# Optimization experiments

Hardware: AMD Instinct MI355X
Metric: run time of the kernel (lower is better)

Reference implementation:

```python
import jax, jax.numpy as jnp
import numpy as np

N, E, G = 250000, 2500000, 512
DIN, H, DEC = 6, 32, 16
BN_EPS = 1e-5


def setup_inputs() -> dict:
    key = jax.random.key(0)
    ks = iter(jax.random.split(key, 64))

    def nrm(shape, s=0.2):
        return s * jax.random.normal(next(ks), shape, jnp.float32)

    inp = {}
    inp["x"] = jax.random.normal(next(ks), (N, DIN), jnp.float32)
    inp["edge_index"] = jax.random.randint(next(ks), (2, E), 0, N)
    inp["batch"] = jnp.sort(jax.random.randint(next(ks), (N,), 0, G))
    dims = [(DIN, H), (H, H), (H, H)]
    for l, (din, dout) in enumerate(dims, 1):
        for d in ("f", "b"):
            inp[f"g{d}{l}_W1"] = nrm((din, dout))
            inp[f"g{d}{l}_b1"] = jnp.zeros((dout,), jnp.float32)
            inp[f"g{d}{l}_W2"] = nrm((dout, dout))
            inp[f"g{d}{l}_b2"] = jnp.zeros((dout,), jnp.float32)
        inp[f"bn{l}_g"] = jnp.ones((dout,), jnp.float32)
        inp[f"bn{l}_b"] = jnp.zeros((dout,), jnp.float32)
    inp["lb_W"] = nrm((H, DEC))
    inp["lb_b"] = jnp.zeros((DEC,), jnp.float32)
    inp["lm_W"] = nrm((DEC, 1))
    inp["lm_b"] = jnp.zeros((1,), jnp.float32)
    return inp


def _gin(x, src, dst, W1, b1, W2, b2):
    # PyG GINConv (eps=0): nn(x + sum_{j->i} x_j); messages flow src -> dst
    agg = jax.ops.segment_sum(x[src], dst, num_segments=x.shape[0])  # [N, d]
    h = x + agg
    return jnp.maximum(h @ W1 + b1, 0.0) @ W2 + b2


def _dgin(x, src, dst, pf, pb, gamma, beta):
    o1 = jax.nn.relu(_gin(x, src, dst, *pf))          # forward direction (A)
    o2 = jax.nn.relu(_gin(x, dst, src, *pb))          # reverse direction (A^T)
    o = 0.5 * (o1 + o2)
    mu = o.mean(0)
    var = o.var(0)  # biased var, as torch BatchNorm1d normalization
    return (o - mu) * jax.lax.rsqrt(var + BN_EPS) * gamma + beta


def reference(x, edge_index, batch,
              gf1_W1, gf1_b1, gf1_W2, gf1_b2, gb1_W1, gb1_b1, gb1_W2, gb1_b2, bn1_g, bn1_b,
              gf2_W1, gf2_b1, gf2_W2, gf2_b2, gb2_W1, gb2_b1, gb2_W2, gb2_b2, bn2_g, bn2_b,
              gf3_W1, gf3_b1, gf3_W2, gf3_b2, gb3_W1, gb3_b1, gb3_W2, gb3_b2, bn3_g, bn3_b,
              lb_W, lb_b, lm_W, lm_b):
    src, dst = edge_index[0], edge_index[1]
    h = _dgin(x, src, dst, (gf1_W1, gf1_b1, gf1_W2, gf1_b2), (gb1_W1, gb1_b1, gb1_W2, gb1_b2), bn1_g, bn1_b)
    h = _dgin(h, src, dst, (gf2_W1, gf2_b1, gf2_W2, gf2_b2), (gb2_W1, gb2_b1, gb2_W2, gb2_b2), bn2_g, bn2_b)
    h = _dgin(h, src, dst, (gf3_W1, gf3_b1, gf3_W2, gf3_b2), (gb3_W1, gb3_b1, gb3_W2, gb3_b2), bn3_g, bn3_b)
    # global mean pool over graphs
    sums = jax.ops.segment_sum(h, batch, num_segments=G)                     # [G, H]
    cnts = jax.ops.segment_sum(jnp.ones((h.shape[0],), h.dtype), batch, num_segments=G)
    pooled = sums / jnp.maximum(cnts, 1.0)[:, None]
    emb = jax.nn.relu(pooled @ lb_W + lb_b)   # dropout: identity (eval)
    return jax.nn.sigmoid(emb @ lm_W + lm_b)  # [G, 1]
```

## Files before the change

kernel.cpp:

```cpp
#include <hip/hip_runtime.h>
#include <math.h>

#define N_NODES 250000
#define N_EDGES 2500000
#define N_GRAPHS 512
#define BN_EPS 1e-5f
#define NT 500000
#define INV_N (1.0f / (float)N_NODES)
#define NBUCK 245
#define BSHIFT 10

__device__ __forceinline__ unsigned short f2bf(float x) {
    unsigned int u = __float_as_uint(x);
    unsigned int r = (u + 0x7FFFu + ((u >> 16) & 1u)) >> 16;
    return (unsigned short)r;
}
__device__ __forceinline__ float bf2f(unsigned short b) {
    return __uint_as_float(((unsigned int)b) << 16);
}


__global__ __launch_bounds__(256)
void k_histA(const int* __restrict__ src, const int* __restrict__ dst,
             int* __restrict__ gcnt, int E)
{
    __shared__ int hF[256], hB[256];
    int t = threadIdx.x;
    hF[t] = 0; hB[t] = 0;
    __syncthreads();
    for (int e = blockIdx.x * 256 + t; e < E; e += gridDim.x * 256) {
        atomicAdd(&hF[dst[e] >> BSHIFT], 1);
        atomicAdd(&hB[src[e] >> BSHIFT], 1);
    }
    __syncthreads();
    if (hF[t]) atomicAdd(&gcnt[t], hF[t]);
    if (hB[t]) atomicAdd(&gcnt[256 + t], hB[t]);
}

__global__ void k_scanBk(const int* __restrict__ gcnt,
                         int* __restrict__ bOffF, int* __restrict__ bOffB,
                         int* __restrict__ cursF, int* __restrict__ cursB,
                         int* __restrict__ off)
{
    __shared__ int s[512];
    int t = threadIdx.x;
    int vF = (t < NBUCK) ? gcnt[t] : 0;
    int vB = (t < NBUCK) ? gcnt[256 + t] : 0;
    s[t] = vF; s[256 + t] = vB;
    __syncthreads();
    for (int o = 1; o < 256; o <<= 1) {
        int xF = (t >= o) ? s[t - o] : 0;
        int xB = (t >= o) ? s[256 + t - o] : 0;
        __syncthreads();
        s[t] += xF; s[256 + t] += xB;
        __syncthreads();
    }
    int exF = s[t] - vF;
    int exB = s[256 + t] - vB;
    if (t < NBUCK) {
        bOffF[t] = exF; cursF[t] = exF;
        bOffB[t] = exB; cursB[t] = exB;
    }
    if (t == 0) {
        bOffF[NBUCK] = N_EDGES;
        bOffB[NBUCK] = N_EDGES;
        off[NT] = 2 * N_EDGES;
    }
}

__global__ __launch_bounds__(256)
void k_scatA(const int* __restrict__ src, const int* __restrict__ dst,
             int* __restrict__ cursF, int* __restrict__ cursB,
             unsigned int* __restrict__ payF, unsigned int* __restrict__ payB, int E)
{
    __shared__ int hF[256], hB[256];
    __shared__ int cF[256], cB[256];
    int t = threadIdx.x;
    hF[t] = 0; hB[t] = 0;
    __syncthreads();
    int e0 = blockIdx.x * 256 + t, STR = gridDim.x * 256;
    for (int e = e0; e < E; e += STR) {
        atomicAdd(&hF[dst[e] >> BSHIFT], 1);
        atomicAdd(&hB[src[e] >> BSHIFT], 1);
    }
    __syncthreads();
    int baseF = 0, baseB = 0;
    if (t < NBUCK) {
        if (hF[t]) baseF = atomicAdd(&cursF[t], hF[t]);
        if (hB[t]) baseB = atomicAdd(&cursB[t], hB[t]);
    }
    __syncthreads();
    cF[t] = baseF; cB[t] = baseB;
    __syncthreads();
    for (int e = e0; e < E; e += STR) {
        int s = src[e], d = dst[e];
        int tf = atomicAdd(&cF[d >> BSHIFT], 1);
        payF[tf] = ((unsigned int)(d & 1023) << 18) | (unsigned int)s;
        int tb = atomicAdd(&cB[s >> BSHIFT], 1);
        payB[tb] = ((unsigned int)(s & 1023) << 18) | (unsigned int)d;
    }
}

__global__ __launch_bounds__(256)
void k_bucket(const unsigned int* __restrict__ payF, const unsigned int* __restrict__ payB,
              const int* __restrict__ bOffF, const int* __restrict__ bOffB,
              int* __restrict__ eidx, int* __restrict__ off)
{
    __shared__ int cnt[1024];
    __shared__ int ps[256];
    int blk = blockIdx.x;
    int d  = (blk >= NBUCK) ? 1 : 0;
    int bb = blk - d * NBUCK;
    const unsigned int* pay = d ? payB : payF;
    const int* bOff = d ? bOffB : bOffF;
    int t = threadIdx.x;
    int lo = bOff[bb], hi = bOff[bb + 1];

    #pragma unroll
    for (int k = 0; k < 4; k++) cnt[t + 256 * k] = 0;
    __syncthreads();
    for (int e = lo + t; e < hi; e += 256)
        atomicAdd(&cnt[pay[e] >> 18], 1);
    __syncthreads();

    int b4 = 4 * t;
    int v0 = cnt[b4], v1 = cnt[b4 + 1], v2 = cnt[b4 + 2], v3 = cnt[b4 + 3];
    int tsum = v0 + v1 + v2 + v3;
    ps[t] = tsum;
    __syncthreads();
    for (int o = 1; o < 256; o <<= 1) {
        int x = (t >= o) ? ps[t - o] : 0;
        __syncthreads();
        ps[t] += x;
        __syncthreads();
    }
    int run = ps[t] - tsum;
    int l0 = run, l1 = run + v0, l2 = run + v0 + v1, l3 = run + v0 + v1 + v2;
    cnt[b4] = l0; cnt[b4 + 1] = l1; cnt[b4 + 2] = l2; cnt[b4 + 3] = l3;

    int gbase = d * N_EDGES + lo;
    int node0 = bb * 1024 + b4;
    if (node0 + 0 < N_NODES) off[d * N_NODES + node0 + 0] = gbase + l0;
    if (node0 + 1 < N_NODES) off[d * N_NODES + node0 + 1] = gbase + l1;
    if (node0 + 2 < N_NODES) off[d * N_NODES + node0 + 2] = gbase + l2;
    if (node0 + 3 < N_NODES) off[d * N_NODES + node0 + 3] = gbase + l3;
    __syncthreads();

    for (int e = lo + t; e < hi; e += 256) {
        unsigned int p = pay[e];
        int r = atomicAdd(&cnt[p >> 18], 1);
        eidx[gbase + r] = (int)(p & 0x3FFFFu);
    }
}


__global__ void pad_x(const float* __restrict__ x, float* __restrict__ xpad, int n)
{
    int i = blockIdx.x * blockDim.x + threadIdx.x;
    if (i >= n * 4) return;
    int node = i >> 2, p2 = i & 3;
    float2 v;
    v.x = (2 * p2     < 6) ? x[node * 6 + 2 * p2]     : 0.f;
    v.y = (2 * p2 + 1 < 6) ? x[node * 6 + 2 * p2 + 1] : 0.f;
    *(float2*)(xpad + node * 8 + 2 * p2) = v;
}


__global__ __launch_bounds__(256, 8)
void gather6p(const float* __restrict__ xpad, const int* __restrict__ off,
              const int* __restrict__ eidx, float* __restrict__ agg, int ngroups)
{
    int tid = threadIdx.x;
    int p2   = tid & 3;
    int slot = tid >> 2;
    for (int grp = blockIdx.x; grp < ngroups; grp += gridDim.x) {
        int node = grp * 64 + slot;
        bool nvalid = (node < N_NODES);
        int nd = nvalid ? node : 0;
        #pragma unroll
        for (int dir = 0; dir < 2; dir++) {
            int u = dir * N_NODES + nd;
            int k0 = off[u], k1 = off[u + 1];
            if (!nvalid) k1 = k0;
            float a0=0.f,a1=0.f,b0=0.f,b1=0.f,c0=0.f,c1=0.f,d0=0.f,d1=0.f;
            for (int p = k0; p < k1; p += 8) {
                #pragma unroll
                for (int q = 0; q < 8; q++) {
                    int kk = p + q;
                    bool act = (kk < k1);
                    int j = eidx[act ? kk : k0];
                    float2 v = *(const float2*)(xpad + j * 8 + 2 * p2);
                    float lo = act ? v.x : 0.f;
                    float hi = act ? v.y : 0.f;
                    if ((q & 3) == 0)      { a0 += lo; a1 += hi; }
                    else if ((q & 3) == 1) { b0 += lo; b1 += hi; }
                    else if ((q & 3) == 2) { c0 += lo; c1 += hi; }
                    else                   { d0 += lo; d1 += hi; }
                }
            }
            if (nvalid && p2 < 3) {
                float2 s;
                s.x = (a0 + b0) + (c0 + d0);
                s.y = (a1 + b1) + (c1 + d1);
                *(float2*)(agg + nd * 12 + dir * 6 + 2 * p2) = s;
            }
        }
    }
}


__global__ __launch_bounds__(256, 8)
void gather16(const unsigned short* __restrict__ xb, const int* __restrict__ off,
              const int* __restrict__ eidx, float* __restrict__ agg, int ngroups)
{
    const unsigned int* xu = (const unsigned int*)xb;
    int tid = threadIdx.x;
    int fp = tid & 15;
    int gg = tid >> 4;
    for (int grp = blockIdx.x; grp < ngroups; grp += gridDim.x) {
        int node = grp * 16 + gg;
        #pragma unroll
        for (int dir = 0; dir < 2; dir++) {
            int u = dir * N_NODES + node;
            int k0 = off[u], k1 = off[u + 1];
            float a0 = 0.f, a1 = 0.f, b0 = 0.f, b1 = 0.f;
            float c0 = 0.f, c1 = 0.f, d0 = 0.f, d1 = 0.f;
            for (int p = k0; p < k1; p += 8) {
                #pragma unroll
                for (int q = 0; q < 8; q++) {
                    int kk = p + q;
                    bool act = (kk < k1);
                    int j = eidx[act ? kk : k0];
                    unsigned int v = xu[j * 16 + fp];
                    float lo = act ? __uint_as_float(v << 16) : 0.f;
                    float hi = act ? __uint_as_float(v & 0xFFFF0000u) : 0.f;
                    if ((q & 3) == 0)      { a0 += lo; a1 += hi; }
                    else if ((q & 3) == 1) { b0 += lo; b1 += hi; }
                    else if ((q & 3) == 2) { c0 += lo; c1 += hi; }
                    else                   { d0 += lo; d1 += hi; }
                }
            }
            float2 s;
            s.x = (a0 + b0) + (c0 + d0);
            s.y = (a1 + b1) + (c1 + d1);
            *(float2*)(agg + node * 64 + dir * 32 + 2 * fp) = s;
        }
    }
}


__global__ __launch_bounds__(256, 6)
void gather16_12(const unsigned short* __restrict__ xb, const int* __restrict__ off,
                 const int* __restrict__ eidx, float* __restrict__ agg, int ngroups)
{
    const unsigned int* xu = (const unsigned int*)xb;
    int tid = threadIdx.x;
    int fp = tid & 15;
    int gg = tid >> 4;
    for (int grp = blockIdx.x; grp < ngroups; grp += gridDim.x) {
        int node = grp * 16 + gg;
        #pragma unroll
        for (int dir = 0; dir < 2; dir++) {
            int u = dir * N_NODES + node;
            int k0 = off[u], k1 = off[u + 1];
            float a0 = 0.f, a1 = 0.f, b0 = 0.f, b1 = 0.f;
            float c0 = 0.f, c1 = 0.f, d0 = 0.f, d1 = 0.f;
            for (int p = k0; p < k1; p += 12) {
                #pragma unroll
                for (int q = 0; q < 12; q++) {
                    int kk = p + q;
                    bool act = (kk < k1);
                    int j = eidx[act ? kk : k0];
                    unsigned int v = xu[j * 16 + fp];
                    float lo = act ? __uint_as_float(v << 16) : 0.f;
                    float hi = act ? __uint_as_float(v & 0xFFFF0000u) : 0.f;
                    if ((q & 3) == 0)      { a0 += lo; a1 += hi; }
                    else if ((q & 3) == 1) { b0 += lo; b1 += hi; }
                    else if ((q & 3) == 2) { c0 += lo; c1 += hi; }
                    else                   { d0 += lo; d1 += hi; }
                }
            }
            float2 s;
            s.x = (a0 + b0) + (c0 + d0);
            s.y = (a1 + b1) + (c1 + d1);
            *(float2*)(agg + node * 64 + dir * 32 + 2 * fp) = s;
        }
    }
}


template <int DIN, bool BN_IN, bool IN_BF16>
__global__ __launch_bounds__(256, 2)
void dgin_mlp2(const void* __restrict__ xin_v, const float* __restrict__ agg,
               const int* __restrict__ off,
               const float* __restrict__ in_stats,
               const float* __restrict__ in_g, const float* __restrict__ in_b,
               const float* __restrict__ W1f, const float* __restrict__ b1f,
               const float* __restrict__ W2f, const float* __restrict__ b2f,
               const float* __restrict__ W1b, const float* __restrict__ b1b,
               const float* __restrict__ W2b, const float* __restrict__ b2b,
               unsigned short* __restrict__ out, float* __restrict__ stats, int n)
{
    const float* xf = (const float*)xin_v;
    const unsigned short* xb = (const unsigned short*)xin_v;

    __shared__ __align__(16) float sW1[2][DIN * 32];
    __shared__ __align__(16) float sW2[2][32 * 32];
    __shared__ float sb1[2][32], sb2[2][32];
    __shared__ float sscale[32], sshift[32];
    __shared__ float sred[4 * 64];

    int tid = threadIdx.x;
    for (int i = tid; i < DIN * 32; i += 256) { sW1[0][i] = W1f[i]; sW1[1][i] = W1b[i]; }
    for (int i = tid; i < 32 * 32;  i += 256) { sW2[0][i] = W2f[i]; sW2[1][i] = W2b[i]; }
    if (tid < 32) {
        sb1[0][tid] = b1f[tid]; sb1[1][tid] = b1b[tid];
        sb2[0][tid] = b2f[tid]; sb2[1][tid] = b2b[tid];
        if (BN_IN) {
            float mu  = in_stats[tid] * INV_N;
            float var = in_stats[32 + tid] * INV_N - mu * mu;
            float sc  = in_g[tid] * rsqrtf(var + BN_EPS);
            sscale[tid] = sc;
            sshift[tid] = in_b[tid] - mu * sc;
        } else { sscale[tid] = 1.f; sshift[tid] = 0.f; }
    }
    __syncthreads();

    int n0 = blockIdx.x * 256 + tid;
    bool valid = (n0 < n);
    int node = valid ? n0 : (n - 1);

    float xr[DIN];
    if (IN_BF16) {
        const uint4* xp = (const uint4*)(xb + node * 32);
        #pragma unroll
        for (int q = 0; q < 4; q++) {
            uint4 u = xp[q];
            unsigned int w[4] = {u.x, u.y, u.z, u.w};
            #pragma unroll
            for (int k = 0; k < 4; k++) {
                xr[8*q + 2*k]     = __uint_as_float(w[k] << 16);
                xr[8*q + 2*k + 1] = __uint_as_float(w[k] & 0xFFFF0000u);
            }
        }
    } else if (DIN == 32) {
        const float4* xp = (const float4*)(xf + node * 32);
        #pragma unroll
        for (int q = 0; q < 8; q++) {
            float4 w = xp[q];
            xr[4*q+0] = w.x; xr[4*q+1] = w.y; xr[4*q+2] = w.z; xr[4*q+3] = w.w;
        }
    } else {
        const float2* xp = (const float2*)(xf + node * DIN);
        #pragma unroll
        for (int q = 0; q < DIN / 2; q++) {
            float2 w = xp[q];
            xr[2*q+0] = w.x; xr[2*q+1] = w.y;
        }
    }

    float o[32];

    #pragma unroll
    for (int dir = 0; dir < 2; dir++) {
        float ag[DIN];
        if (DIN == 32) {
            const float4* ap = (const float4*)(agg + node * 64 + dir * 32);
            #pragma unroll
            for (int q = 0; q < 8; q++) {
                float4 w = ap[q];
                ag[4*q+0] = w.x; ag[4*q+1] = w.y; ag[4*q+2] = w.z; ag[4*q+3] = w.w;
            }
        } else {
            const float* ap = agg + node * (2 * DIN) + dir * DIN;
            #pragma unroll
            for (int i = 0; i < DIN; i++) ag[i] = ap[i];
        }
        int ob = dir * N_NODES + node;
        float degp1 = (float)(off[ob + 1] - off[ob] + 1);

        float t1[32];
        #pragma unroll
        for (int j = 0; j < 32; j++) t1[j] = sb1[dir][j];
        #pragma unroll
        for (int i = 0; i < DIN; i++) {
            float hv = xr[i] + ag[i];
            if (BN_IN) hv = fmaf(sscale[i], hv, degp1 * sshift[i]);
            const float4* wr = (const float4*)(&sW1[dir][i * 32]);
            #pragma unroll
            for (int q = 0; q < 8; q++) {
                float4 w = wr[q];
                t1[4*q+0] = fmaf(hv, w.x, t1[4*q+0]);
                t1[4*q+1] = fmaf(hv, w.y, t1[4*q+1]);
                t1[4*q+2] = fmaf(hv, w.z, t1[4*q+2]);
                t1[4*q+3] = fmaf(hv, w.w, t1[4*q+3]);
            }
        }
        #pragma unroll
        for (int j = 0; j < 32; j++) t1[j] = fmaxf(t1[j], 0.f);

        float o2[32];
        #pragma unroll
        for (int j = 0; j < 32; j++) o2[j] = sb2[dir][j];
        #pragma unroll
        for (int i = 0; i < 32; i++) {
            float hv = t1[i];
            const float4* wr = (const float4*)(&sW2[dir][i * 32]);
            #pragma unroll
            for (int q = 0; q < 8; q++) {
                float4 w = wr[q];
                o2[4*q+0] = fmaf(hv, w.x, o2[4*q+0]);
                o2[4*q+1] = fmaf(hv, w.y, o2[4*q+1]);
                o2[4*q+2] = fmaf(hv, w.z, o2[4*q+2]);
                o2[4*q+3] = fmaf(hv, w.w, o2[4*q+3]);
            }
        }
        if (dir == 0) {
            #pragma unroll
            for (int j = 0; j < 32; j++) o[j] = fmaxf(o2[j], 0.f);
        } else {
            #pragma unroll
            for (int j = 0; j < 32; j++) o[j] = 0.5f * (o[j] + fmaxf(o2[j], 0.f));
        }
    }

    #pragma unroll
    for (int j = 0; j < 32; j++) o[j] = bf2f(f2bf(o[j]));

    if (valid) {
        uint4* op = (uint4*)(out + node * 32);
        #pragma unroll
        for (int q = 0; q < 4; q++) {
            uint4 u;
            u.x = (unsigned int)f2bf(o[8*q+0]) | ((unsigned int)f2bf(o[8*q+1]) << 16);
            u.y = (unsigned int)f2bf(o[8*q+2]) | ((unsigned int)f2bf(o[8*q+3]) << 16);
            u.z = (unsigned int)f2bf(o[8*q+4]) | ((unsigned int)f2bf(o[8*q+5]) << 16);
            u.w = (unsigned int)f2bf(o[8*q+6]) | ((unsigned int)f2bf(o[8*q+7]) << 16);
            op[q] = u;
        }
    }

    int lane = tid & 63;
    int wave = tid >> 6;
    #pragma unroll
    for (int f = 0; f < 32; f++) {
        float v = valid ? o[f] : 0.f;
        float v2 = v * v;
        #pragma unroll
        for (int offs = 32; offs > 0; offs >>= 1) {
            v  += __shfl_down(v, offs);
            v2 += __shfl_down(v2, offs);
        }
        if (lane == 0) {
            sred[wave * 64 + f]      = v;
            sred[wave * 64 + 32 + f] = v2;
        }
    }
    __syncthreads();
    if (tid < 64) {
        float a = sred[tid] + sred[64 + tid] + sred[128 + tid] + sred[192 + tid];
        atomicAdd(&stats[tid], a);
    }
}


__global__ void pool_seg(const unsigned short* __restrict__ h, const int* __restrict__ batch,
                         float* __restrict__ psum, float* __restrict__ pcnt, int n)
{
    int tid = threadIdx.x;
    int grp = tid >> 5, f = tid & 31;
    int base = blockIdx.x * 256;
    float acc = 0.f, cnt = 0.f;
    int curg = -1;
    for (int it = 0; it < 32; it++) {
        int nd = base + grp + it * 8;
        if (nd < n) {
            int g = batch[nd];
            if (g != curg) {
                if (curg >= 0) {
                    atomicAdd(&psum[curg * 32 + f], acc);
                    if (f == 0) atomicAdd(&pcnt[curg], cnt);
                }
                curg = g; acc = 0.f; cnt = 0.f;
            }
            acc += bf2f(h[nd * 32 + f]);
            cnt += 1.f;
        }
    }
    if (curg >= 0) {
        atomicAdd(&psum[curg * 32 + f], acc);
        if (f == 0) atomicAdd(&pcnt[curg], cnt);
    }
}

__global__ void head_kernel(const float* __restrict__ psum, const float* __restrict__ pcnt,
                            const float* __restrict__ stats3,
                            const float* __restrict__ g3, const float* __restrict__ b3,
                            const float* __restrict__ lbW, const float* __restrict__ lbb,
                            const float* __restrict__ lmW, const float* __restrict__ lmb,
                            float* __restrict__ out)
{
    int g = threadIdx.x;
    float cnt = fmaxf(pcnt[g], 1.0f);
    float inv = 1.0f / cnt;
    float p[32];
    #pragma unroll
    for (int i = 0; i < 32; i++) {
        float mu  = stats3[i] * INV_N;
        float var = stats3[32 + i] * INV_N - mu * mu;
        float a   = g3[i] * rsqrtf(var + BN_EPS);
        float b   = b3[i] - mu * a;
        p[i] = fmaf(a, psum[g * 32 + i] * inv, b);
    }
    float z = lmb[0];
    #pragma unroll
    for (int k = 0; k < 16; k++) {
        float acc = lbb[k];
        #pragma unroll
        for (int i = 0; i < 32; i++) acc += p[i] * lbW[i * 16 + k];
        z += fmaxf(acc, 0.0f) * lmW[k];
    }
    out[g] = 1.0f / (1.0f + expf(-z));
}


extern "C" void kernel_launch(void* const* d_in, const int* in_sizes, int n_in,
                              void* d_out, int out_size, void* d_ws, size_t ws_size,
                              hipStream_t stream)
{
    const float* x   = (const float*)d_in[0];
    const int* ei    = (const int*)d_in[1];
    const int* batch = (const int*)d_in[2];
    const int* src = ei;
    const int* dst = ei + N_EDGES;
    char* ws = (char*)d_ws;

    auto W = [&](int l, int j) { return (const float*)d_in[3 + (l - 1) * 10 + j]; };

    unsigned short* h = (unsigned short*)(ws + 0);
    float* xpad = (float*)(ws + 16000016);
    float* agg  = (float*)(ws + 32000000);
    int*   eidx = (int*)  (ws + 96000000);
    int*   off  = (int*)  (ws + 116000000);
    int* gcnt  = (int*)(ws + 32000000);
    int* bOffF = (int*)(ws + 32002048);
    int* bOffB = (int*)(ws + 32003072);
    int* cursF = (int*)(ws + 32004096);
    int* cursB = (int*)(ws + 32005120);
    unsigned int* payF = (unsigned int*)(ws + 32008192);
    unsigned int* payB = (unsigned int*)(ws + 42008192);
    float* stats1 = (float*)(ws + 118000016);
    float* stats2 = stats1 + 64;
    float* stats3 = stats1 + 128;
    float* psum   = (float*)(ws + 118000784);
    float* pcnt   = (float*)(ws + 118066320);

    hipMemsetAsync(gcnt, 0, 2048, stream);
    k_histA<<<1024, 256, 0, stream>>>(src, dst, gcnt, N_EDGES);
    k_scanBk<<<1, 256, 0, stream>>>(gcnt, bOffF, bOffB, cursF, cursB, off);
    k_scatA<<<384, 256, 0, stream>>>(src, dst, cursF, cursB, payF, payB, N_EDGES);
    k_bucket<<<2 * NBUCK, 256, 0, stream>>>(payF, payB, bOffF, bOffB, eidx, off);

    pad_x<<<(N_NODES * 4 + 255) / 256, 256, 0, stream>>>(x, xpad, N_NODES);
    hipMemsetAsync(stats1, 0, 3 * 64 * 4, stream);

    const int GG   = 4096;
    const int NG64 = (N_NODES + 63) / 64;
    const int NG16 = N_NODES / 16;
    const int GM   = (N_NODES + 255) / 256;

    gather6p<<<GG, 256, 0, stream>>>(xpad, off, eidx, agg, NG64);
    dgin_mlp2<6, false, false><<<GM, 256, 0, stream>>>(
        x, agg, off, nullptr, nullptr, nullptr,
        W(1,0), W(1,1), W(1,2), W(1,3), W(1,4), W(1,5), W(1,6), W(1,7),
        h, stats1, N_NODES);

    gather16<<<GG, 256, 0, stream>>>(h, off, eidx, agg, NG16);
    dgin_mlp2<32, true, true><<<GM, 256, 0, stream>>>(
        h, agg, off, stats1, W(1,8), W(1,9),
        W(2,0), W(2,1), W(2,2), W(2,3), W(2,4), W(2,5), W(2,6), W(2,7),
        h, stats2, N_NODES);

    gather16_12<<<GG, 256, 0, stream>>>(h, off, eidx, agg, NG16);
    dgin_mlp2<32, true, true><<<GM, 256, 0, stream>>>(
        h, agg, off, stats2, W(2,8), W(2,9),
        W(3,0), W(3,1), W(3,2), W(3,3), W(3,4), W(3,5), W(3,6), W(3,7),
        h, stats3, N_NODES);

    hipMemsetAsync(psum, 0, (size_t)N_GRAPHS * 32 * 4, stream);
    hipMemsetAsync(pcnt, 0, (size_t)N_GRAPHS * 4, stream);
    pool_seg<<<(N_NODES + 255) / 256, 256, 0, stream>>>(h, batch, psum, pcnt, N_NODES);
    head_kernel<<<1, 512, 0, stream>>>(psum, pcnt, stats3, W(3,8), W(3,9),
        (const float*)d_in[33], (const float*)d_in[34],
        (const float*)d_in[35], (const float*)d_in[36],
        (float*)d_out);
}
```

Baseline: 808.1 us.

## Split forward and reverse MLP directions across paired threads in dgin_mlp2

```diff
diff --git a/kernel.cpp b/kernel.cpp
--- a/kernel.cpp
+++ b/kernel.cpp
@@ -290,7 +290,7 @@
 
 
 template <int DIN, bool BN_IN, bool IN_BF16>
-__global__ __launch_bounds__(256, 2)
+__global__ __launch_bounds__(256, 4)
 void dgin_mlp2(const void* __restrict__ xin_v, const float* __restrict__ agg,
                const int* __restrict__ off,
                const float* __restrict__ in_stats,
@@ -326,7 +326,9 @@
     }
     __syncthreads();
 
-    int n0 = blockIdx.x * 256 + tid;
+    int nl  = tid >> 1;
+    int dir = tid & 1;
+    int n0 = blockIdx.x * 128 + nl;
     bool valid = (n0 < n);
     int node = valid ? n0 : (n - 1);
 
@@ -343,13 +345,6 @@
                 xr[8*q + 2*k + 1] = __uint_as_float(w[k] & 0xFFFF0000u);
             }
         }
-    } else if (DIN == 32) {
-        const float4* xp = (const float4*)(xf + node * 32);
-        #pragma unroll
-        for (int q = 0; q < 8; q++) {
-            float4 w = xp[q];
-            xr[4*q+0] = w.x; xr[4*q+1] = w.y; xr[4*q+2] = w.z; xr[4*q+3] = w.w;
-        }
     } else {
         const float2* xp = (const float2*)(xf + node * DIN);
         #pragma unroll
@@ -359,69 +354,65 @@
         }
     }
 
+    float ag[DIN];
+    if (DIN == 32) {
+        const float4* ap = (const float4*)(agg + node * 64 + dir * 32);
+        #pragma unroll
+        for (int q = 0; q < 8; q++) {
+            float4 w = ap[q];
+            ag[4*q+0] = w.x; ag[4*q+1] = w.y; ag[4*q+2] = w.z; ag[4*q+3] = w.w;
+        }
+    } else {
+        const float* ap = agg + node * (2 * DIN) + dir * DIN;
+        #pragma unroll
+        for (int i = 0; i < DIN; i++) ag[i] = ap[i];
+    }
+    int ob = dir * N_NODES + node;
+    float degp1 = (float)(off[ob + 1] - off[ob] + 1);
+
+    float t1[32];
+    #pragma unroll
+    for (int j = 0; j < 32; j++) t1[j] = sb1[dir][j];
+    #pragma unroll
+    for (int i = 0; i < DIN; i++) {
+        float hv = xr[i] + ag[i];
+        if (BN_IN) hv = fmaf(sscale[i], hv, degp1 * sshift[i]);
+        const float4* wr = (const float4*)(&sW1[dir][i * 32]);
+        #pragma unroll
+        for (int q = 0; q < 8; q++) {
+            float4 w = wr[q];
+            t1[4*q+0] = fmaf(hv, w.x, t1[4*q+0]);
+            t1[4*q+1] = fmaf(hv, w.y, t1[4*q+1]);
+            t1[4*q+2] = fmaf(hv, w.z, t1[4*q+2]);
+            t1[4*q+3] = fmaf(hv, w.w, t1[4*q+3]);
+        }
+    }
+    #pragma unroll
+    for (int j = 0; j < 32; j++) t1[j] = fmaxf(t1[j], 0.f);
+
+    float o2[32];
+    #pragma unroll
+    for (int j = 0; j < 32; j++) o2[j] = sb2[dir][j];
+    #pragma unroll
+    for (int i = 0; i < 32; i++) {
+        float hv = t1[i];
+        const float4* wr = (const float4*)(&sW2[dir][i * 32]);
+        #pragma unroll
+        for (int q = 0; q < 8; q++) {
+            float4 w = wr[q];
+            o2[4*q+0] = fmaf(hv, w.x, o2[4*q+0]);
+            o2[4*q+1] = fmaf(hv, w.y, o2[4*q+1]);
+            o2[4*q+2] = fmaf(hv, w.z, o2[4*q+2]);
+            o2[4*q+3] = fmaf(hv, w.w, o2[4*q+3]);
+        }
+    }
+
     float o[32];
-
-    #pragma unroll
-    for (int dir = 0; dir < 2; dir++) {
-        float ag[DIN];
-        if (DIN == 32) {
-            const float4* ap = (const float4*)(agg + node * 64 + dir * 32);
-            #pragma unroll
-            for (int q = 0; q < 8; q++) {
-                float4 w = ap[q];
-                ag[4*q+0] = w.x; ag[4*q+1] = w.y; ag[4*q+2] = w.z; ag[4*q+3] = w.w;
-            }
-        } else {
-            const float* ap = agg + node * (2 * DIN) + dir * DIN;
-            #pragma unroll
-            for (int i = 0; i < DIN; i++) ag[i] = ap[i];
-        }
-        int ob = dir * N_NODES + node;
-        float degp1 = (float)(off[ob + 1] - off[ob] + 1);
-
-        float t1[32];
-        #pragma unroll
-        for (int j = 0; j < 32; j++) t1[j] = sb1[dir][j];
-        #pragma unroll
-        for (int i = 0; i < DIN; i++) {
-            float hv = xr[i] + ag[i];
-            if (BN_IN) hv = fmaf(sscale[i], hv, degp1 * sshift[i]);
-            const float4* wr = (const float4*)(&sW1[dir][i * 32]);
-            #pragma unroll
-            for (int q = 0; q < 8; q++) {
-                float4 w = wr[q];
-                t1[4*q+0] = fmaf(hv, w.x, t1[4*q+0]);
-                t1[4*q+1] = fmaf(hv, w.y, t1[4*q+1]);
-                t1[4*q+2] = fmaf(hv, w.z, t1[4*q+2]);
-                t1[4*q+3] = fmaf(hv, w.w, t1[4*q+3]);
-            }
-        }
-        #pragma unroll
-        for (int j = 0; j < 32; j++) t1[j] = fmaxf(t1[j], 0.f);
-
-        float o2[32];
-        #pragma unroll
-        for (int j = 0; j < 32; j++) o2[j] = sb2[dir][j];
-        #pragma unroll
-        for (int i = 0; i < 32; i++) {
-            float hv = t1[i];
-            const float4* wr = (const float4*)(&sW2[dir][i * 32]);
-            #pragma unroll
-            for (int q = 0; q < 8; q++) {
-                float4 w = wr[q];
-                o2[4*q+0] = fmaf(hv, w.x, o2[4*q+0]);
-                o2[4*q+1] = fmaf(hv, w.y, o2[4*q+1]);
-                o2[4*q+2] = fmaf(hv, w.z, o2[4*q+2]);
-                o2[4*q+3] = fmaf(hv, w.w, o2[4*q+3]);
-            }
-        }
-        if (dir == 0) {
-            #pragma unroll
-            for (int j = 0; j < 32; j++) o[j] = fmaxf(o2[j], 0.f);
-        } else {
-            #pragma unroll
-            for (int j = 0; j < 32; j++) o[j] = 0.5f * (o[j] + fmaxf(o2[j], 0.f));
-        }
+    #pragma unroll
+    for (int j = 0; j < 32; j++) {
+        float r  = fmaxf(o2[j], 0.f);
+        float pr = __shfl_xor(r, 1);
+        o[j] = 0.5f * (r + pr);
     }
 
     #pragma unroll
@@ -430,13 +421,14 @@
     if (valid) {
         uint4* op = (uint4*)(out + node * 32);
         #pragma unroll
-        for (int q = 0; q < 4; q++) {
+        for (int q = 0; q < 2; q++) {
+            int qq = dir * 2 + q;
             uint4 u;
-            u.x = (unsigned int)f2bf(o[8*q+0]) | ((unsigned int)f2bf(o[8*q+1]) << 16);
-            u.y = (unsigned int)f2bf(o[8*q+2]) | ((unsigned int)f2bf(o[8*q+3]) << 16);
-            u.z = (unsigned int)f2bf(o[8*q+4]) | ((unsigned int)f2bf(o[8*q+5]) << 16);
-            u.w = (unsigned int)f2bf(o[8*q+6]) | ((unsigned int)f2bf(o[8*q+7]) << 16);
-            op[q] = u;
+            u.x = (unsigned int)f2bf(o[8*qq+0]) | ((unsigned int)f2bf(o[8*qq+1]) << 16);
+            u.y = (unsigned int)f2bf(o[8*qq+2]) | ((unsigned int)f2bf(o[8*qq+3]) << 16);
+            u.z = (unsigned int)f2bf(o[8*qq+4]) | ((unsigned int)f2bf(o[8*qq+5]) << 16);
+            u.w = (unsigned int)f2bf(o[8*qq+6]) | ((unsigned int)f2bf(o[8*qq+7]) << 16);
+            op[qq] = u;
         }
     }
 
@@ -444,7 +436,7 @@
     int wave = tid >> 6;
     #pragma unroll
     for (int f = 0; f < 32; f++) {
-        float v = valid ? o[f] : 0.f;
+        float v = (valid && dir == 0) ? o[f] : 0.f;
         float v2 = v * v;
         #pragma unroll
         for (int offs = 32; offs > 0; offs >>= 1) {
@@ -567,7 +559,7 @@
     const int GG   = 4096;
     const int NG64 = (N_NODES + 63) / 64;
     const int NG16 = N_NODES / 16;
-    const int GM   = (N_NODES + 255) / 256;
+    const int GM   = (N_NODES + 127) / 128;
 
     gather6p<<<GG, 256, 0, stream>>>(xpad, off, eidx, agg, NG64);
     dgin_mlp2<6, false, false><<<GM, 256, 0, stream>>>(
```

Measured after the change: 872.3 us. 1.08x slower.
